# Kernel optimization log

Measured on AMD Instinct MI355X. Metric: run time of the kernel, lower is better.

The kernel has to match this reference:

```python
import jax, jax.numpy as jnp
import numpy as np

B, T, H = 128, 2048, 128

def setup_inputs() -> dict:
    key = jax.random.key(0)
    k1, k2, k3, k4, k5, k6 = jax.random.split(key, 6)
    s = 1.0 / np.sqrt(H)
    return {
        "H_pos": jax.random.normal(k1, (B, T, H), jnp.float32),
        "H_dyn": jax.random.normal(k2, (B, T, H), jnp.float32),
        "acc_w": jax.random.uniform(k3, (B, T), jnp.float32),
        "W_h": jax.random.uniform(k4, (H, H), jnp.float32, -s, s),
        "W_d": jax.random.uniform(k5, (H, H), jnp.float32, -s, s),
        "W_a": jax.random.uniform(k6, (H,), jnp.float32, -s, s),
        "b_a": jnp.zeros((), jnp.float32),
        "beta": jnp.zeros((), jnp.float32),
    }

def reference(H_pos, H_dyn, acc_w, W_h, W_d, W_a, b_a, beta):
    # energy: W_a(tanh(W_h H_pos + W_d H_dyn)) -> [B, T]
    z = jnp.tanh(jnp.einsum('bth,oh->bto', H_pos, W_h)
                 + jnp.einsum('bth,oh->bto', H_dyn, W_d))
    energy = jnp.einsum('bth,h->bt', z, W_a) + b_a
    # acceleration normalization
    acc_norm = acc_w / jnp.clip(jnp.max(acc_w, axis=1, keepdims=True), 1e-6)
    beta_pos = jax.nn.softplus(beta)
    alpha = jax.nn.softmax(energy * (1.0 + beta_pos * acc_norm), axis=1)  # [B, T]
    context = jnp.einsum('bt,bth->bh', alpha, H_pos)  # [B, H]
    return (context, alpha)
```

## Files before the change

kernel.cpp:

```cpp
#include <hip/hip_runtime.h>

#define B_ 128
#define T_ 2048
#define H_ 128
#define WPAD 136

typedef __attribute__((ext_vector_type(8))) short short8;
typedef __attribute__((ext_vector_type(4))) float f32x4;

__device__ __forceinline__ unsigned short f2b(float f) {
    unsigned int u = __float_as_uint(f);
    u += 0x7fffu + ((u >> 16) & 1u);
    return (unsigned short)(u >> 16);
}
__device__ __forceinline__ short8 pack8(const float4 x, const float4 y) {
    short8 r;
    r[0] = (short)f2b(x.x); r[1] = (short)f2b(x.y);
    r[2] = (short)f2b(x.z); r[3] = (short)f2b(x.w);
    r[4] = (short)f2b(y.x); r[5] = (short)f2b(y.y);
    r[6] = (short)f2b(y.z); r[7] = (short)f2b(y.w);
    return r;
}
__device__ __forceinline__ float tanh_fast(float x) {
    x = fminf(fmaxf(x, -20.f), 20.f);
    float e = __expf(2.f * x);
    return (e - 1.f) / (e + 1.f);
}

__global__ __launch_bounds__(512) void energy_kernel(
    const float* __restrict__ Hp,
    const float* __restrict__ Hd,
    const float* __restrict__ Wh,
    const float* __restrict__ Wd,
    const float* __restrict__ Wa,
    const float* __restrict__ ba_p,
    float* __restrict__ energy,
    int ntiles)
{
    __shared__ unsigned short Whs[H_ * WPAD];
    __shared__ unsigned short Wds[H_ * WPAD];
    __shared__ float Was[H_];

    const int tid = threadIdx.x;

    for (int i = tid; i < (H_ * H_) / 4; i += 512) {
        int row = i >> 5;
        int c4  = (i & 31) * 4;
        float4 wh = *(const float4*)&Wh[row * H_ + c4];
        float4 wd = *(const float4*)&Wd[row * H_ + c4];
        uint2 ph, pd;
        ph.x = (unsigned)f2b(wh.x) | ((unsigned)f2b(wh.y) << 16);
        ph.y = (unsigned)f2b(wh.z) | ((unsigned)f2b(wh.w) << 16);
        pd.x = (unsigned)f2b(wd.x) | ((unsigned)f2b(wd.y) << 16);
        pd.y = (unsigned)f2b(wd.z) | ((unsigned)f2b(wd.w) << 16);
        *(uint2*)&Whs[row * WPAD + c4] = ph;
        *(uint2*)&Wds[row * WPAD + c4] = pd;
    }
    if (tid < H_) Was[tid] = Wa[tid];
    __syncthreads();

    const float ba = ba_p[0];

    const int wave = tid >> 6;
    const int lane = tid & 63;
    const int l15  = lane & 15;
    const int lq   = lane >> 4;

    for (int tile = blockIdx.x; tile < ntiles; tile += gridDim.x) {
        const int row_base = tile * 128 + wave * 16;
        const float* ap = Hp + (size_t)(row_base + l15) * H_ + lq * 8;
        const float* ad = Hd + (size_t)(row_base + l15) * H_ + lq * 8;

        f32x4 acc[8];
        #pragma unroll
        for (int nt = 0; nt < 8; nt++) acc[nt] = (f32x4){0.f, 0.f, 0.f, 0.f};

        float4 cx0 = *(const float4*)(ap);
        float4 cx1 = *(const float4*)(ap + 4);

        #pragma unroll 1
        for (int kt = 0; kt < 8; kt++) {
            float4 nx0 = cx0, nx1 = cx1;
            if (kt < 7) {
                int ktn = kt + 1;
                const float* pn = (ktn < 4) ? (ap + ktn * 32) : (ad + (ktn - 4) * 32);
                nx0 = *(const float4*)pn;
                nx1 = *(const float4*)(pn + 4);
            }
            short8 af = pack8(cx0, cx1);
            const unsigned short* ws = (kt < 4) ? Whs : Wds;
            const int kk = (kt & 3) * 32 + lq * 8;
            #pragma unroll
            for (int nt = 0; nt < 8; nt++) {
                short8 bf = *(const short8*)&ws[(nt * 16 + l15) * WPAD + kk];
                acc[nt] = __builtin_amdgcn_mfma_f32_16x16x32_bf16(af, bf, acc[nt], 0, 0, 0);
            }
            cx0 = nx0; cx1 = nx1;
        }

        float ep[4] = {0.f, 0.f, 0.f, 0.f};
        #pragma unroll
        for (int nt = 0; nt < 8; nt++) {
            const float wa = Was[nt * 16 + l15];
            #pragma unroll
            for (int r = 0; r < 4; r++) ep[r] += tanh_fast(acc[nt][r]) * wa;
        }
        #pragma unroll
        for (int m = 1; m < 16; m <<= 1) {
            #pragma unroll
            for (int r = 0; r < 4; r++) ep[r] += __shfl_xor(ep[r], m, 64);
        }
        if (l15 == 0) {
            #pragma unroll
            for (int r = 0; r < 4; r++)
                energy[row_base + lq * 4 + r] = ep[r] + ba;
        }
    }
}

__global__ __launch_bounds__(256) void softmax_ctx_kernel(
    const float* __restrict__ Hp,
    const float* __restrict__ accw,
    const float* __restrict__ beta_p,
    const float* __restrict__ energy,
    float* __restrict__ out_alpha,
    float* __restrict__ cpart)
{
    __shared__ float al_s[T_];
    __shared__ float red[8 * H_];
    __shared__ float sred[8];

    const int sl   = blockIdx.x & 7;
    const int b    = blockIdx.x >> 3;
    const int tid  = threadIdx.x;
    const int lane = tid & 63;
    const int wid  = tid >> 6;

    const float beta_pos = log1pf(__expf(beta_p[0]));

    float av[8], ev[8];
    {
        const float* pa = accw + b * T_ + tid * 8;
        const float* pe = energy + b * T_ + tid * 8;
        float4 a0 = *(const float4*)pa, a1 = *(const float4*)(pa + 4);
        float4 e0 = *(const float4*)pe, e1 = *(const float4*)(pe + 4);
        av[0]=a0.x; av[1]=a0.y; av[2]=a0.z; av[3]=a0.w;
        av[4]=a1.x; av[5]=a1.y; av[6]=a1.z; av[7]=a1.w;
        ev[0]=e0.x; ev[1]=e0.y; ev[2]=e0.z; ev[3]=e0.w;
        ev[4]=e1.x; ev[5]=e1.y; ev[6]=e1.z; ev[7]=e1.w;
    }
    float amax = -1e30f;
    #pragma unroll
    for (int i = 0; i < 8; i++) amax = fmaxf(amax, av[i]);
    for (int m = 32; m >= 1; m >>= 1) amax = fmaxf(amax, __shfl_xor(amax, m, 64));
    if (lane == 0) sred[wid] = amax;
    __syncthreads();
    if (tid == 0)
        sred[4] = fmaxf(fmaxf(sred[0], sred[1]), fmaxf(sred[2], sred[3]));
    __syncthreads();
    const float invd = beta_pos / fmaxf(sred[4], 1e-6f);

    float sv[8], smax = -1e30f;
    #pragma unroll
    for (int i = 0; i < 8; i++) {
        sv[i] = ev[i] * (1.f + av[i] * invd);
        smax = fmaxf(smax, sv[i]);
    }
    for (int m = 32; m >= 1; m >>= 1) smax = fmaxf(smax, __shfl_xor(smax, m, 64));
    __syncthreads();
    if (lane == 0) sred[wid] = smax;
    __syncthreads();
    if (tid == 0)
        sred[5] = fmaxf(fmaxf(sred[0], sred[1]), fmaxf(sred[2], sred[3]));
    __syncthreads();
    const float smax_all = sred[5];

    float p[8], psum = 0.f;
    #pragma unroll
    for (int i = 0; i < 8; i++) { p[i] = __expf(sv[i] - smax_all); psum += p[i]; }
    for (int m = 32; m >= 1; m >>= 1) psum += __shfl_xor(psum, m, 64);
    __syncthreads();
    if (lane == 0) sred[wid] = psum;
    __syncthreads();
    if (tid == 0)
        sred[6] = sred[0] + sred[1] + sred[2] + sred[3];
    __syncthreads();
    const float invS = 1.f / sred[6];

    #pragma unroll
    for (int i = 0; i < 8; i++) al_s[tid * 8 + i] = p[i] * invS;
    __syncthreads();

    out_alpha[b * T_ + sl * 256 + tid] = al_s[sl * 256 + tid];

    const int row = tid >> 5;
    const int c4  = tid & 31;

    float c0 = 0.f, c1 = 0.f, c2 = 0.f, c3 = 0.f;
    const float* base = Hp + ((size_t)b * T_ + sl * 256) * H_ + c4 * 4;
    const float* al   = al_s + sl * 256;
    #pragma unroll 4
    for (int it = 0; it < 32; it++) {
        int t = it * 8 + row;
        float a = al[t];
        float4 v = *(const float4*)(base + (size_t)t * H_);
        c0 += a * v.x; c1 += a * v.y; c2 += a * v.z; c3 += a * v.w;
    }
    red[row * H_ + c4 * 4 + 0] = c0;
    red[row * H_ + c4 * 4 + 1] = c1;
    red[row * H_ + c4 * 4 + 2] = c2;
    red[row * H_ + c4 * 4 + 3] = c3;
    __syncthreads();
    if (tid < H_) {
        float s = 0.f;
        #pragma unroll
        for (int g = 0; g < 8; g++) s += red[g * H_ + tid];
        cpart[(b * 8 + sl) * H_ + tid] = s;
    }
}

__global__ __launch_bounds__(256) void ctx_reduce_kernel(
    const float* __restrict__ cpart, float* __restrict__ out_ctx)
{
    int i = blockIdx.x * 256 + threadIdx.x;
    if (i < B_ * H_) {
        int b = i >> 7, h = i & 127;
        float s = 0.f;
        #pragma unroll
        for (int g = 0; g < 8; g++) s += cpart[(b * 8 + g) * H_ + h];
        out_ctx[i] = s;
    }
}

extern "C" void kernel_launch(void* const* d_in, const int* in_sizes, int n_in,
                              void* d_out, int out_size, void* d_ws, size_t ws_size,
                              hipStream_t stream) {
    const float* Hp   = (const float*)d_in[0];
    const float* Hd   = (const float*)d_in[1];
    const float* accw = (const float*)d_in[2];
    const float* Wh   = (const float*)d_in[3];
    const float* Wd   = (const float*)d_in[4];
    const float* Wa   = (const float*)d_in[5];
    const float* ba   = (const float*)d_in[6];
    const float* beta = (const float*)d_in[7];

    float* energy_ws = (float*)d_ws;
    float* cpart_ws  = energy_ws + B_ * T_;

    float* out_ctx   = (float*)d_out;
    float* out_alpha = out_ctx + B_ * H_;

    const int ntiles = (B_ * T_) / 128;
    energy_kernel<<<512, 512, 0, stream>>>(Hp, Hd, Wh, Wd, Wa, ba, energy_ws, ntiles);
    softmax_ctx_kernel<<<B_ * 8, 256, 0, stream>>>(Hp, accw, beta, energy_ws, out_alpha, cpart_ws);
    ctx_reduce_kernel<<<(B_ * H_ + 255) / 256, 256, 0, stream>>>(cpart_ws, out_ctx);
}
```

Before: 318.4 us.

## Pre-swizzle weight fragments, double rows per wave, split context over 16 slices

The energy kernel now stores the bf16 weights in LDS already arranged in MFMA B-fragment order, so each lane reads contiguously without padding. Each wave handles 32 rows instead of 16, so every B fragment loaded from LDS feeds two MFMAs. The softmax/context kernel splits each batch row into 16 slices of 128 timesteps instead of 8, with four independent accumulators, to give more blocks and more loads in flight. In exchange, each of the 16 blocks per batch row recomputes the full-row softmax, the energy kernel uses more registers, and the reduction kernel reads twice as many partials.

```diff
diff --git a/kernel.cpp b/kernel.cpp
--- a/kernel.cpp
+++ b/kernel.cpp
@@ -1,25 +1,20 @@
 #include <hip/hip_runtime.h>
+#include <hip/hip_bf16.h>
 
 #define B_ 128
 #define T_ 2048
 #define H_ 128
-#define WPAD 136
 
 typedef __attribute__((ext_vector_type(8))) short short8;
 typedef __attribute__((ext_vector_type(4))) float f32x4;
 
-__device__ __forceinline__ unsigned short f2b(float f) {
-    unsigned int u = __float_as_uint(f);
-    u += 0x7fffu + ((u >> 16) & 1u);
-    return (unsigned short)(u >> 16);
-}
 __device__ __forceinline__ short8 pack8(const float4 x, const float4 y) {
-    short8 r;
-    r[0] = (short)f2b(x.x); r[1] = (short)f2b(x.y);
-    r[2] = (short)f2b(x.z); r[3] = (short)f2b(x.w);
-    r[4] = (short)f2b(y.x); r[5] = (short)f2b(y.y);
-    r[6] = (short)f2b(y.z); r[7] = (short)f2b(y.w);
-    return r;
+    union { __hip_bfloat162 h2[4]; short8 s; } u;
+    u.h2[0] = __float22bfloat162_rn(make_float2(x.x, x.y));
+    u.h2[1] = __float22bfloat162_rn(make_float2(x.z, x.w));
+    u.h2[2] = __float22bfloat162_rn(make_float2(y.x, y.y));
+    u.h2[3] = __float22bfloat162_rn(make_float2(y.z, y.w));
+    return u.s;
 }
 __device__ __forceinline__ float tanh_fast(float x) {
     x = fminf(fmaxf(x, -20.f), 20.f);
@@ -37,24 +32,23 @@
     float* __restrict__ energy,
     int ntiles)
 {
-    __shared__ unsigned short Whs[H_ * WPAD];
-    __shared__ unsigned short Wds[H_ * WPAD];
+    __shared__ unsigned short Bfrag[64 * 64 * 8];
     __shared__ float Was[H_];
 
     const int tid = threadIdx.x;
 
-    for (int i = tid; i < (H_ * H_) / 4; i += 512) {
-        int row = i >> 5;
-        int c4  = (i & 31) * 4;
-        float4 wh = *(const float4*)&Wh[row * H_ + c4];
-        float4 wd = *(const float4*)&Wd[row * H_ + c4];
-        uint2 ph, pd;
-        ph.x = (unsigned)f2b(wh.x) | ((unsigned)f2b(wh.y) << 16);
-        ph.y = (unsigned)f2b(wh.z) | ((unsigned)f2b(wh.w) << 16);
-        pd.x = (unsigned)f2b(wd.x) | ((unsigned)f2b(wd.y) << 16);
-        pd.y = (unsigned)f2b(wd.z) | ((unsigned)f2b(wd.w) << 16);
-        *(uint2*)&Whs[row * WPAD + c4] = ph;
-        *(uint2*)&Wds[row * WPAD + c4] = pd;
+    #pragma unroll
+    for (int p = 0; p < 8; p++) {
+        int fl = p * 512 + tid;
+        int f  = fl >> 6;
+        int l  = fl & 63;
+        int kt = f >> 3, nt = f & 7;
+        int o   = nt * 16 + (l & 15);
+        int col = kt * 32 + ((l >> 4) << 3);
+        const float* src = (kt < 4) ? (Wh + o * H_ + col) : (Wd + o * H_ + (col - 128));
+        float4 x0 = *(const float4*)src;
+        float4 x1 = *(const float4*)(src + 4);
+        *(short8*)&Bfrag[fl * 8] = pack8(x0, x1);
     }
     if (tid < H_) Was[tid] = Wa[tid];
     __syncthreads();
@@ -67,53 +61,69 @@
     const int lq   = lane >> 4;
 
     for (int tile = blockIdx.x; tile < ntiles; tile += gridDim.x) {
-        const int row_base = tile * 128 + wave * 16;
-        const float* ap = Hp + (size_t)(row_base + l15) * H_ + lq * 8;
-        const float* ad = Hd + (size_t)(row_base + l15) * H_ + lq * 8;
-
-        f32x4 acc[8];
-        #pragma unroll
-        for (int nt = 0; nt < 8; nt++) acc[nt] = (f32x4){0.f, 0.f, 0.f, 0.f};
-
-        float4 cx0 = *(const float4*)(ap);
-        float4 cx1 = *(const float4*)(ap + 4);
+        const int row0 = tile * 256 + wave * 32;
+        const float* a0p = Hp + (size_t)(row0 + l15) * H_ + lq * 8;
+        const float* a1p = a0p + 16 * H_;
+        const float* a0d = Hd + (size_t)(row0 + l15) * H_ + lq * 8;
+        const float* a1d = a0d + 16 * H_;
+
+        f32x4 acc0[8], acc1[8];
+        #pragma unroll
+        for (int nt = 0; nt < 8; nt++) {
+            acc0[nt] = (f32x4){0.f, 0.f, 0.f, 0.f};
+            acc1[nt] = (f32x4){0.f, 0.f, 0.f, 0.f};
+        }
+
+        float4 p00 = *(const float4*)(a0p), p01 = *(const float4*)(a0p + 4);
+        float4 p10 = *(const float4*)(a1p), p11 = *(const float4*)(a1p + 4);
 
         #pragma unroll 1
         for (int kt = 0; kt < 8; kt++) {
-            float4 nx0 = cx0, nx1 = cx1;
+            float4 n00 = p00, n01 = p01, n10 = p10, n11 = p11;
             if (kt < 7) {
                 int ktn = kt + 1;
-                const float* pn = (ktn < 4) ? (ap + ktn * 32) : (ad + (ktn - 4) * 32);
-                nx0 = *(const float4*)pn;
-                nx1 = *(const float4*)(pn + 4);
-            }
-            short8 af = pack8(cx0, cx1);
-            const unsigned short* ws = (kt < 4) ? Whs : Wds;
-            const int kk = (kt & 3) * 32 + lq * 8;
+                const float* q0 = (ktn < 4) ? (a0p + ktn * 32) : (a0d + (ktn - 4) * 32);
+                const float* q1 = (ktn < 4) ? (a1p + ktn * 32) : (a1d + (ktn - 4) * 32);
+                n00 = *(const float4*)q0; n01 = *(const float4*)(q0 + 4);
+                n10 = *(const float4*)q1; n11 = *(const float4*)(q1 + 4);
+            }
+            short8 af0 = pack8(p00, p01);
+            short8 af1 = pack8(p10, p11);
+            const unsigned short* bp = &Bfrag[kt * 8 * 512 + lane * 8];
             #pragma unroll
             for (int nt = 0; nt < 8; nt++) {
-                short8 bf = *(const short8*)&ws[(nt * 16 + l15) * WPAD + kk];
-                acc[nt] = __builtin_amdgcn_mfma_f32_16x16x32_bf16(af, bf, acc[nt], 0, 0, 0);
-            }
-            cx0 = nx0; cx1 = nx1;
-        }
-
-        float ep[4] = {0.f, 0.f, 0.f, 0.f};
+                short8 bf = *(const short8*)(bp + nt * 512);
+                acc0[nt] = __builtin_amdgcn_mfma_f32_16x16x32_bf16(af0, bf, acc0[nt], 0, 0, 0);
+                acc1[nt] = __builtin_amdgcn_mfma_f32_16x16x32_bf16(af1, bf, acc1[nt], 0, 0, 0);
+            }
+            p00 = n00; p01 = n01; p10 = n10; p11 = n11;
+        }
+
+        float ep0[4] = {0.f, 0.f, 0.f, 0.f};
+        float ep1[4] = {0.f, 0.f, 0.f, 0.f};
         #pragma unroll
         for (int nt = 0; nt < 8; nt++) {
             const float wa = Was[nt * 16 + l15];
             #pragma unroll
-            for (int r = 0; r < 4; r++) ep[r] += tanh_fast(acc[nt][r]) * wa;
+            for (int r = 0; r < 4; r++) {
+                ep0[r] += tanh_fast(acc0[nt][r]) * wa;
+                ep1[r] += tanh_fast(acc1[nt][r]) * wa;
+            }
         }
         #pragma unroll
         for (int m = 1; m < 16; m <<= 1) {
             #pragma unroll
-            for (int r = 0; r < 4; r++) ep[r] += __shfl_xor(ep[r], m, 64);
+            for (int r = 0; r < 4; r++) {
+                ep0[r] += __shfl_xor(ep0[r], m, 64);
+                ep1[r] += __shfl_xor(ep1[r], m, 64);
+            }
         }
         if (l15 == 0) {
             #pragma unroll
-            for (int r = 0; r < 4; r++)
-                energy[row_base + lq * 4 + r] = ep[r] + ba;
+            for (int r = 0; r < 4; r++) {
+                energy[row0 + lq * 4 + r]      = ep0[r] + ba;
+                energy[row0 + 16 + lq * 4 + r] = ep1[r] + ba;
+            }
         }
     }
 }
@@ -130,8 +140,8 @@
     __shared__ float red[8 * H_];
     __shared__ float sred[8];
 
-    const int sl   = blockIdx.x & 7;
-    const int b    = blockIdx.x >> 3;
+    const int sl   = blockIdx.x & 15;
+    const int b    = blockIdx.x >> 4;
     const int tid  = threadIdx.x;
     const int lane = tid & 63;
     const int wid  = tid >> 6;
@@ -191,31 +201,45 @@
     for (int i = 0; i < 8; i++) al_s[tid * 8 + i] = p[i] * invS;
     __syncthreads();
 
-    out_alpha[b * T_ + sl * 256 + tid] = al_s[sl * 256 + tid];
+    if (tid < 128)
+        out_alpha[b * T_ + sl * 128 + tid] = al_s[sl * 128 + tid];
 
     const int row = tid >> 5;
     const int c4  = tid & 31;
 
-    float c0 = 0.f, c1 = 0.f, c2 = 0.f, c3 = 0.f;
-    const float* base = Hp + ((size_t)b * T_ + sl * 256) * H_ + c4 * 4;
-    const float* al   = al_s + sl * 256;
-    #pragma unroll 4
-    for (int it = 0; it < 32; it++) {
-        int t = it * 8 + row;
-        float a = al[t];
-        float4 v = *(const float4*)(base + (size_t)t * H_);
-        c0 += a * v.x; c1 += a * v.y; c2 += a * v.z; c3 += a * v.w;
-    }
-    red[row * H_ + c4 * 4 + 0] = c0;
-    red[row * H_ + c4 * 4 + 1] = c1;
-    red[row * H_ + c4 * 4 + 2] = c2;
-    red[row * H_ + c4 * 4 + 3] = c3;
+    const float* base = Hp + ((size_t)b * T_ + sl * 128) * H_ + c4 * 4;
+    const float* al   = al_s + sl * 128;
+
+    float4 s0 = {0,0,0,0}, s1 = {0,0,0,0}, s2 = {0,0,0,0}, s3 = {0,0,0,0};
+    #pragma unroll
+    for (int it = 0; it < 16; it += 4) {
+        int t0 = (it + 0) * 8 + row, t1 = (it + 1) * 8 + row;
+        int t2 = (it + 2) * 8 + row, t3 = (it + 3) * 8 + row;
+        float a0 = al[t0], a1 = al[t1], a2 = al[t2], a3 = al[t3];
+        float4 v0 = *(const float4*)(base + (size_t)t0 * H_);
+        float4 v1 = *(const float4*)(base + (size_t)t1 * H_);
+        float4 v2 = *(const float4*)(base + (size_t)t2 * H_);
+        float4 v3 = *(const float4*)(base + (size_t)t3 * H_);
+        s0.x += a0*v0.x; s0.y += a0*v0.y; s0.z += a0*v0.z; s0.w += a0*v0.w;
+        s1.x += a1*v1.x; s1.y += a1*v1.y; s1.z += a1*v1.z; s1.w += a1*v1.w;
+        s2.x += a2*v2.x; s2.y += a2*v2.y; s2.z += a2*v2.z; s2.w += a2*v2.w;
+        s3.x += a3*v3.x; s3.y += a3*v3.y; s3.z += a3*v3.z; s3.w += a3*v3.w;
+    }
+    s0.x += s1.x + s2.x + s3.x;
+    s0.y += s1.y + s2.y + s3.y;
+    s0.z += s1.z + s2.z + s3.z;
+    s0.w += s1.w + s2.w + s3.w;
+
+    red[row * H_ + c4 * 4 + 0] = s0.x;
+    red[row * H_ + c4 * 4 + 1] = s0.y;
+    red[row * H_ + c4 * 4 + 2] = s0.z;
+    red[row * H_ + c4 * 4 + 3] = s0.w;
     __syncthreads();
     if (tid < H_) {
         float s = 0.f;
         #pragma unroll
         for (int g = 0; g < 8; g++) s += red[g * H_ + tid];
-        cpart[(b * 8 + sl) * H_ + tid] = s;
+        cpart[(b * 16 + sl) * H_ + tid] = s;
     }
 }
 
@@ -227,7 +251,7 @@
         int b = i >> 7, h = i & 127;
         float s = 0.f;
         #pragma unroll
-        for (int g = 0; g < 8; g++) s += cpart[(b * 8 + g) * H_ + h];
+        for (int g = 0; g < 16; g++) s += cpart[(b * 16 + g) * H_ + h];
         out_ctx[i] = s;
     }
 }
@@ -250,8 +274,8 @@
     float* out_ctx   = (float*)d_out;
     float* out_alpha = out_ctx + B_ * H_;
 
-    const int ntiles = (B_ * T_) / 128;
+    const int ntiles = (B_ * T_) / 256;
     energy_kernel<<<512, 512, 0, stream>>>(Hp, Hd, Wh, Wd, Wa, ba, energy_ws, ntiles);
-    softmax_ctx_kernel<<<B_ * 8, 256, 0, stream>>>(Hp, accw, beta, energy_ws, out_alpha, cpart_ws);
+    softmax_ctx_kernel<<<B_ * 16, 256, 0, stream>>>(Hp, accw, beta, energy_ws, out_alpha, cpart_ws);
     ctx_reduce_kernel<<<(B_ * H_ + 255) / 256, 256, 0, stream>>>(cpart_ws, out_ctx);
 }
```

Measured after the change: 322.3 us. No clear change (+1.2%).
